# Kernel optimization log

Measured on AMD Instinct MI355X. Metric: run time of the kernel, lower is better.

## Reference

```python
import jax, jax.numpy as jnp
import numpy as np

HID, DIN, ORDER = 64, 1, 2
EPS = 1e-5


def conv1x1(x, W, b):
    # x: [b, c_in, n] -> [b, c_out, n]
    return jnp.einsum('oi,bin->bon', W, x) + b[:, None]


def gconv(x, supports, W, b, order, include_self):
    outs = [x] if include_self else []
    for A in supports:
        x1 = jnp.einsum('bcv,wv->bcw', x, A)
        outs.append(x1)
        for _ in range(order - 1):
            x1 = jnp.einsum('bcv,wv->bcw', x1, A)
            outs.append(x1)
    return conv1x1(jnp.concatenate(outs, axis=1), W, b)


def _forward(x, mask, adj, h0, fs_W, fs_b, li_W, li_b, gc_W, gc_b, lo_W, lo_b,
             ro_W, ro_b, prelu_a, f_W, f_b, u_W, u_b, c_W, c_b, gn_g, gn_beta):
    B = x.shape[0]
    supports = [adj[0], adj[1]]
    h = jnp.broadcast_to(h0, (B,) + h0.shape)  # [b, HID, n]

    def step(h, inp):
        x_s, m_s = inp  # [b, DIN, n] each
        mbool = m_s > 0
        # first stage prediction from hidden state
        xs_hat_1 = conv1x1(h, fs_W, fs_b)
        x1 = jnp.where(mbool, x_s, xs_hat_1)
        # spatial decoder (order=1, no attention)
        x_in = conv1x1(jnp.concatenate([x1, m_s, h], axis=1), li_W, li_b)
        out = gconv(x_in, supports, gc_W, gc_b, order=1, include_self=False)
        out = conv1x1(jnp.concatenate([out, h], axis=1), lo_W, lo_b)
        out = jnp.where(out >= 0, out, prelu_a * out)  # PReLU
        repr_s = jnp.concatenate([out, h], axis=1)     # [b, 2*HID, n]
        xs_hat_2 = conv1x1(repr_s, ro_W, ro_b)
        x2 = jnp.where(mbool, x1, xs_hat_2)
        # GCGRU cell (order-2 graph conv gates, include_self=True)
        rnn_in = jnp.concatenate([x2, m_s], axis=1)    # [b, 2*DIN, n]
        xh = jnp.concatenate([rnn_in, h], axis=1)
        r = jax.nn.sigmoid(gconv(xh, supports, f_W, f_b, ORDER, True))
        u = jax.nn.sigmoid(gconv(xh, supports, u_W, u_b, ORDER, True))
        xc = jnp.concatenate([rnn_in, r * h], axis=1)
        c = jnp.tanh(gconv(xc, supports, c_W, c_b, ORDER, True))
        h_new = u * h + (1.0 - u) * c
        # GroupNorm(num_groups=1): normalize over (C, N) per sample
        mu = h_new.mean(axis=(1, 2), keepdims=True)
        var = h_new.var(axis=(1, 2), keepdims=True)
        h_n = (h_new - mu) / jnp.sqrt(var + EPS) * gn_g[:, None] + gn_beta[:, None]
        return h_n, (xs_hat_2, xs_hat_1, h_n, repr_s)

    xs = jnp.moveaxis(x, -1, 0)     # [T, b, DIN, n]
    ms = jnp.moveaxis(mask, -1, 0)
    _, (imp, pred, states, reprs) = jax.lax.scan(step, h, (xs, ms))
    imputations = jnp.moveaxis(imp, 0, -1)          # [b, DIN, n, T]
    predictions = jnp.moveaxis(pred, 0, -1)
    states = jnp.moveaxis(states, 0, -1)[None]      # [n_layers=1, b, HID, n, T]
    representations = jnp.moveaxis(reprs, 0, -1)    # [b, 2*HID, n, T]
    return imputations, predictions, representations, states


def setup_inputs() -> dict:
    key = jax.random.key(0)
    ks = jax.random.split(key, 24)
    B, N, T = 8, 1024, 24
    rnn_in = 2 * DIN                 # x + mask
    dec_in = rnn_in + HID            # 66
    gate_in = 5 * (rnn_in + HID)     # (order*support_len + self) * (d_in + hidden)

    def w(k, o, i):
        return (jax.random.normal(k, (o, i), jnp.float32) / np.sqrt(i)).astype(jnp.float32)

    x = jax.random.normal(ks[0], (B, DIN, N, T), jnp.float32)
    mask = jax.random.bernoulli(ks[1], 0.8, (B, DIN, N, T)).astype(jnp.float32)
    A = jax.random.uniform(ks[2], (N, N), jnp.float32)
    A = A * (A > 0.97)  # sparse-ish graph
    fwd = A / (A.sum(1, keepdims=True) + 1e-8)
    bwd = A.T / (A.T.sum(1, keepdims=True) + 1e-8)
    adj = jnp.stack([fwd, bwd])
    return {
        'x': x, 'mask': mask, 'adj': adj,
        'h0': jax.random.normal(ks[3], (HID, N), jnp.float32) / np.sqrt(HID),
        'fs_W': w(ks[4], DIN, HID), 'fs_b': jnp.zeros((DIN,), jnp.float32),
        'li_W': w(ks[5], HID, dec_in), 'li_b': jnp.zeros((HID,), jnp.float32),
        'gc_W': w(ks[6], HID, 2 * HID), 'gc_b': jnp.zeros((HID,), jnp.float32),
        'lo_W': w(ks[7], HID, 2 * HID), 'lo_b': jnp.zeros((HID,), jnp.float32),
        'ro_W': w(ks[8], DIN, 2 * HID), 'ro_b': jnp.zeros((DIN,), jnp.float32),
        'prelu_a': jnp.float32(0.25),
        'f_W': w(ks[9], HID, gate_in), 'f_b': jnp.zeros((HID,), jnp.float32),
        'u_W': w(ks[10], HID, gate_in), 'u_b': jnp.zeros((HID,), jnp.float32),
        'c_W': w(ks[11], HID, gate_in), 'c_b': jnp.zeros((HID,), jnp.float32),
        'gn_g': jnp.ones((HID,), jnp.float32), 'gn_beta': jnp.zeros((HID,), jnp.float32),
    }


def reference(x, mask, adj, h0, fs_W, fs_b, li_W, li_b, gc_W, gc_b, lo_W, lo_b,
              ro_W, ro_b, prelu_a, f_W, f_b, u_W, u_b, c_W, c_b, gn_g, gn_beta):
    return _forward(x, mask, adj, h0, fs_W, fs_b, li_W, li_b, gc_W, gc_b,
                    lo_W, lo_b, ro_W, ro_b, prelu_a, f_W, f_b, u_W, u_b,
                    c_W, c_b, gn_g, gn_beta)
```

## Files before the change

### kernel.cpp

```cpp
#include <hip/hip_runtime.h>
#include <hip/hip_bf16.h>

typedef __hip_bfloat16 bf16;

constexpr int NV=1024, TT=24, BB=8, CAP=80;

constexpr int O_CVAL = 0;
constexpr int O_CIDX = 163840;
constexpr int O_CCNT = 327680;
constexpr int O_LIWT = 329728;
constexpr int O_GCWT = 333952;
constexpr int O_LOWT = 342144;
constexpr int O_FWT  = 350336;
constexpr int O_UWT  = 371456;
constexpr int O_CWT  = 392576;
constexpr int O_H    = 413696;
constexpr int O_T1   = 937984;
constexpr int O_T3   = 1986560;
constexpr int O_XH   = 2510848;
constexpr int O_Z1F  = 3067904;
constexpr int O_Z1B  = 3624960;
constexpr int O_PART = 4182016;
constexpr int O_RST  = 5296144;
constexpr int O_SST  = 17879056;
constexpr size_t WS_FLOATS = 24170512;
constexpr int O_XC = O_T1;
constexpr int O_U  = O_T3;

constexpr int OFF_IMP  = 0;
constexpr int OFF_PRED = 196608;
constexpr int OFF_REPR = 393216;
constexpr int OFF_ST   = 25559040;

__device__ __forceinline__ bf16 f2b(float v){ return __float2bfloat16(v); }
__device__ __forceinline__ float b2f(bf16 v){ return __bfloat162float(v); }

__global__ __launch_bounds__(64) void k_csr(const float* __restrict__ adj, float* __restrict__ ws){
  int row = blockIdx.x, lane = threadIdx.x;
  const float* a = adj + (size_t)row*NV;
  float* val = ws + O_CVAL + (size_t)row*CAP;
  int* idx = (int*)(ws+O_CIDX) + (size_t)row*CAP;
  int count = 0;
  for(int ch=0; ch<NV/64; ++ch){
    float v = a[ch*64+lane];
    unsigned long long m = __ballot(v != 0.f);
    int pre = __popcll(m & ((1ull<<lane)-1ull));
    if(v != 0.f){ int p = count+pre; if(p<CAP){ idx[p]=ch*64+lane; val[p]=v; } }
    count += __popcll(m);
  }
  if(lane==0) ((int*)(ws+O_CCNT))[row] = count>CAP?CAP:count;
}

__global__ void k_prep_wt(const float* __restrict__ liW, const float* __restrict__ gcW,
    const float* __restrict__ loW, const float* __restrict__ fW,
    const float* __restrict__ uW, const float* __restrict__ cW, float* __restrict__ ws){
  int g = blockIdx.x*blockDim.x + threadIdx.x, G = gridDim.x*blockDim.x;
  for(int i=g;i<66*64;i+=G){ int k=i>>6, c=i&63; ws[O_LIWT+i]=liW[c*66+k]; }
  for(int i=g;i<128*64;i+=G){ int k=i>>6, c=i&63; ws[O_GCWT+i]=gcW[c*128+k]; ws[O_LOWT+i]=loW[c*128+k]; }
  for(int i=g;i<330*64;i+=G){ int k=i>>6, c=i&63; ws[O_FWT+i]=fW[c*330+k]; ws[O_UWT+i]=uW[c*330+k]; ws[O_CWT+i]=cW[c*330+k]; }
}

__global__ __launch_bounds__(256) void k_h0(const float* __restrict__ h0, float* __restrict__ ws){
  int g = blockIdx.x*blockDim.x + threadIdx.x;
  if(g >= BB*NV*64) return;
  int c = g&63, n = (g>>6)&1023;
  ws[O_H + g] = h0[c*NV + n];
}

__global__ __launch_bounds__(256) void kA(float* __restrict__ ws,
    const float* __restrict__ x, const float* __restrict__ mask,
    const float* __restrict__ fsW, const float* __restrict__ fsb,
    const float* __restrict__ lib, const float* __restrict__ gng,
    const float* __restrict__ gnb, float* __restrict__ dout, int t){
  __shared__ float hs[4][2][64];
  __shared__ float rs[256], rq[256];
  __shared__ float musd[8][2];
  int tid = threadIdx.x, wid = tid>>6, lane = tid&63;
  int n = blockIdx.x;
  if(t > 0){
    const float2* part = (const float2*)(ws+O_PART);
    for(int b=0;b<8;++b){
      float sx=0.f, sq=0.f;
      for(int i=tid;i<1024;i+=256){ float2 p = part[b*1024+i]; sx+=p.x; sq+=p.y; }
      rs[tid]=sx; rq[tid]=sq; __syncthreads();
      for(int s=128;s;s>>=1){ if(tid<s){ rs[tid]+=rs[tid+s]; rq[tid]+=rq[tid+s]; } __syncthreads(); }
      if(tid==0){ float mu=rs[0]*(1.f/65536.f); float var=rq[0]*(1.f/65536.f)-mu*mu;
                  musd[b][0]=mu; musd[b][1]=rsqrtf(var+1e-5f); }
      __syncthreads();
    }
  }
  float gg = gng[lane], gb = gnb[lane];
  float x1v[2], xmv[2];
  #pragma unroll
  for(int j=0;j<2;++j){
    int b = wid*2+j;
    size_t col = (size_t)(b*NV+n);
    float h = ws[O_H + col*64 + lane];
    if(t > 0){
      h = (h - musd[b][0])*musd[b][1]*gg + gb;
      ws[O_H + col*64 + lane] = h;
      ((bf16*)(ws+O_SST))[(size_t)(t-1)*(BB*NV*64) + col*64 + lane] = f2b(h);
    }
    hs[wid][j][lane] = h;
    float pv = fsW[lane]*h;
    #pragma unroll
    for(int off=32; off; off>>=1) pv += __shfl_xor(pv, off, 64);
    float pred = pv + fsb[0];
    float xm = mask[col*TT + t];
    x1v[j] = (xm>0.f) ? x[col*TT + t] : pred;
    xmv[j] = xm;
    if(lane==0) dout[OFF_PRED + col*TT + t] = pred;
  }
  const float* Wt = ws + O_LIWT;
  float lb = lib[lane];
  float w0 = Wt[lane], w1 = Wt[64+lane];
  float a0 = lb + w0*x1v[0] + w1*xmv[0];
  float a1 = lb + w0*x1v[1] + w1*xmv[1];
  for(int j=0;j<64;++j){
    float w = Wt[(2+j)*64+lane];
    a0 += w*hs[wid][0][j];
    a1 += w*hs[wid][1][j];
  }
  ws[O_T1 + (size_t)((wid*2  )*NV+n)*64 + lane] = a0;
  ws[O_T1 + (size_t)((wid*2+1)*NV+n)*64 + lane] = a1;
}

__global__ __launch_bounds__(256) void kB(float* __restrict__ ws,
    const float* __restrict__ x, const float* __restrict__ mask,
    const float* __restrict__ gcb, const float* __restrict__ lob,
    const float* __restrict__ prelu, const float* __restrict__ roW,
    const float* __restrict__ rob, float* __restrict__ dout, int t){
  __shared__ float pq[4][2][128];
  int tid=threadIdx.x, wid=tid>>6, lane=tid&63;
  int n = blockIdx.x;
  int b0 = wid*2, b1 = wid*2+1;
  const int* ccnt = (const int*)(ws+O_CCNT);
  float p0=0.f,p1=0.f,q0=0.f,q1=0.f;
  {
    int cn = ccnt[n];
    const int* id = (const int*)(ws+O_CIDX) + (size_t)n*CAP;
    const float* vl = ws + O_CVAL + (size_t)n*CAP;
    for(int k=0;k<cn;++k){
      float a = vl[k]; int ix = id[k];
      p0 += a*ws[O_T1 + (size_t)(b0*NV+ix)*64 + lane];
      p1 += a*ws[O_T1 + (size_t)(b1*NV+ix)*64 + lane];
    }
  }
  {
    int cn = ccnt[NV+n];
    const int* id = (const int*)(ws+O_CIDX) + (size_t)(NV+n)*CAP;
    const float* vl = ws + O_CVAL + (size_t)(NV+n)*CAP;
    for(int k=0;k<cn;++k){
      float a = vl[k]; int ix = id[k];
      q0 += a*ws[O_T1 + (size_t)(b0*NV+ix)*64 + lane];
      q1 += a*ws[O_T1 + (size_t)(b1*NV+ix)*64 + lane];
    }
  }
  pq[wid][0][lane]=p0; pq[wid][0][64+lane]=q0;
  pq[wid][1][lane]=p1; pq[wid][1][64+lane]=q1;
  const float* Gt = ws + O_GCWT;
  float g0 = gcb[lane], g1 = g0;
  for(int j=0;j<128;++j){
    float w = Gt[j*64+lane];
    g0 += w*pq[wid][0][j];
    g1 += w*pq[wid][1][j];
  }
  float hv0 = ws[O_H + (size_t)(b0*NV+n)*64 + lane];
  float hv1 = ws[O_H + (size_t)(b1*NV+n)*64 + lane];
  pq[wid][0][lane]=g0; pq[wid][0][64+lane]=hv0;
  pq[wid][1][lane]=g1; pq[wid][1][64+lane]=hv1;
  const float* Lt = ws + O_LOWT;
  float o0 = lob[lane], o1 = o0;
  for(int j=0;j<128;++j){
    float w = Lt[j*64+lane];
    o0 += w*pq[wid][0][j];
    o1 += w*pq[wid][1][j];
  }
  float a = prelu[0];
  float r0 = roW[lane], r1 = roW[64+lane], rb0 = rob[0];
  bf16* reprs = (bf16*)(ws + O_RST);
  #pragma unroll
  for(int j=0;j<2;++j){
    int b = wid*2+j;
    float ov = (j? o1 : o0);
    float hv = (j? hv1 : hv0);
    ov = (ov>=0.f)? ov : a*ov;
    size_t col = (size_t)(b*NV+n);
    size_t rbo = (((size_t)t*BB + b)*NV + n)*128;
    reprs[rbo + lane]      = f2b(ov);
    reprs[rbo + 64 + lane] = f2b(hv);
    float rv = r0*ov + r1*hv;
    #pragma unroll
    for(int off=32; off; off>>=1) rv += __shfl_xor(rv, off, 64);
    float xs2 = rv + rb0;
    float xm = mask[col*TT+t];
    float x2 = (xm>0.f) ? x[col*TT+t] : xs2;
    if(lane==0) dout[OFF_IMP + col*TT + t] = xs2;
    float* xh = ws + O_XH + col*68;
    xh[2+lane] = hv;
    if(lane==0){ xh[0]=x2; xh[1]=xm; }
  }
}

__global__ __launch_bounds__(256) void k_prop(float* __restrict__ ws, int srcF, int srcB,
    int dstF, int dstB){
  int tid=threadIdx.x, wid = tid>>6, lane = tid&63;
  int n = blockIdx.x;
  int b0 = wid*2, b1 = wid*2+1;
  const int* ccnt = (const int*)(ws+O_CCNT);
  bool hi = lane < 2;
  {
    int cn = ccnt[n];
    const int* id = (const int*)(ws+O_CIDX) + (size_t)n*CAP;
    const float* vl = ws + O_CVAL + (size_t)n*CAP;
    float a00=0.f,a01=0.f,a10=0.f,a11=0.f;
    for(int k=0;k<cn;++k){
      float a = vl[k]; int ix = id[k];
      const float* r0 = ws + srcF + (size_t)(b0*NV + ix)*68;
      const float* r1 = ws + srcF + (size_t)(b1*NV + ix)*68;
      a00 += a*r0[lane]; if(hi) a01 += a*r0[64+lane];
      a10 += a*r1[lane]; if(hi) a11 += a*r1[64+lane];
    }
    float* d0 = ws + dstF + (size_t)(b0*NV+n)*68;
    float* d1 = ws + dstF + (size_t)(b1*NV+n)*68;
    d0[lane]=a00; if(hi) d0[64+lane]=a01;
    d1[lane]=a10; if(hi) d1[64+lane]=a11;
  }
  {
    int cn = ccnt[NV+n];
    const int* id = (const int*)(ws+O_CIDX) + (size_t)(NV+n)*CAP;
    const float* vl = ws + O_CVAL + (size_t)(NV+n)*CAP;
    float a00=0.f,a01=0.f,a10=0.f,a11=0.f;
    for(int k=0;k<cn;++k){
      float a = vl[k]; int ix = id[k];
      const float* r0 = ws + srcB + (size_t)(b0*NV + ix)*68;
      const float* r1 = ws + srcB + (size_t)(b1*NV + ix)*68;
      a00 += a*r0[lane]; if(hi) a01 += a*r0[64+lane];
      a10 += a*r1[lane]; if(hi) a11 += a*r1[64+lane];
    }
    float* d0 = ws + dstB + (size_t)(b0*NV+n)*68;
    float* d1 = ws + dstB + (size_t)(b1*NV+n)*68;
    d0[lane]=a00; if(hi) d0[64+lane]=a01;
    d1[lane]=a10; if(hi) d1[64+lane]=a11;
  }
}

__global__ __launch_bounds__(256) void kD(float* __restrict__ ws,
    const float* __restrict__ fb, const float* __restrict__ ub){
  __shared__ float vec[4][2][332];
  int tid=threadIdx.x, wid=tid>>6, lane=tid&63;
  int n = blockIdx.x;
  const int* ccnt = (const int*)(ws+O_CCNT);
  bool hi = lane < 2;
  #pragma unroll
  for(int j=0;j<2;++j){
    size_t col = (size_t)((wid*2+j)*NV+n);
    const float* xh  = ws + O_XH  + col*68;
    const float* z1f = ws + O_Z1F + col*68;
    const float* z1b = ws + O_Z1B + col*68;
    vec[wid][j][lane]     = xh[lane];   if(hi) vec[wid][j][64+lane]  = xh[64+lane];
    vec[wid][j][66+lane]  = z1f[lane];  if(hi) vec[wid][j][130+lane] = z1f[64+lane];
    vec[wid][j][198+lane] = z1b[lane];  if(hi) vec[wid][j][262+lane] = z1b[64+lane];
  }
  {
    int cn = ccnt[n];
    const int* id = (const int*)(ws+O_CIDX) + (size_t)n*CAP;
    const float* vl = ws + O_CVAL + (size_t)n*CAP;
    float a00=0.f,a01=0.f,a10=0.f,a11=0.f;
    for(int k=0;k<cn;++k){
      float a = vl[k]; int ix = id[k];
      const float* r0 = ws + O_Z1F + (size_t)((wid*2  )*NV+ix)*68;
      const float* r1 = ws + O_Z1F + (size_t)((wid*2+1)*NV+ix)*68;
      a00 += a*r0[lane]; if(hi) a01 += a*r0[64+lane];
      a10 += a*r1[lane]; if(hi) a11 += a*r1[64+lane];
    }
    vec[wid][0][132+lane]=a00; if(hi) vec[wid][0][196+lane]=a01;
    vec[wid][1][132+lane]=a10; if(hi) vec[wid][1][196+lane]=a11;
  }
  {
    int cn = ccnt[NV+n];
    const int* id = (const int*)(ws+O_CIDX) + (size_t)(NV+n)*CAP;
    const float* vl = ws + O_CVAL + (size_t)(NV+n)*CAP;
    float a00=0.f,a01=0.f,a10=0.f,a11=0.f;
    for(int k=0;k<cn;++k){
      float a = vl[k]; int ix = id[k];
      const float* r0 = ws + O_Z1B + (size_t)((wid*2  )*NV+ix)*68;
      const float* r1 = ws + O_Z1B + (size_t)((wid*2+1)*NV+ix)*68;
      a00 += a*r0[lane]; if(hi) a01 += a*r0[64+lane];
      a10 += a*r1[lane]; if(hi) a11 += a*r1[64+lane];
    }
    vec[wid][0][264+lane]=a00; if(hi) vec[wid][0][328+lane]=a01;
    vec[wid][1][264+lane]=a10; if(hi) vec[wid][1][328+lane]=a11;
  }
  const float* Ft = ws + O_FWT;
  const float* Ut = ws + O_UWT;
  float ar0 = fb[lane], ar1 = ar0;
  float au0 = ub[lane], au1 = au0;
  for(int k=0;k<330;++k){
    float wf = Ft[k*64+lane];
    float wu = Ut[k*64+lane];
    float v0 = vec[wid][0][k], v1 = vec[wid][1][k];
    ar0 += wf*v0; ar1 += wf*v1;
    au0 += wu*v0; au1 += wu*v1;
  }
  #pragma unroll
  for(int j=0;j<2;++j){
    size_t col = (size_t)((wid*2+j)*NV+n);
    float r = 1.f/(1.f+expf(-(j? ar1 : ar0)));
    float u = 1.f/(1.f+expf(-(j? au1 : au0)));
    float hv = ws[O_H + col*64 + lane];
    ws[O_U + col*64 + lane] = u;
    float* xc = ws + O_XC + col*68;
    xc[2+lane] = r*hv;
    if(hi) xc[lane] = vec[wid][j][lane];
  }
}

__global__ __launch_bounds__(256) void kF(float* __restrict__ ws, const float* __restrict__ cb){
  __shared__ float vec[4][2][332];
  int tid=threadIdx.x, wid=tid>>6, lane=tid&63;
  int n = blockIdx.x;
  const int* ccnt = (const int*)(ws+O_CCNT);
  bool hi = lane < 2;
  #pragma unroll
  for(int j=0;j<2;++j){
    size_t col = (size_t)((wid*2+j)*NV+n);
    const float* xc  = ws + O_XC  + col*68;
    const float* w1f = ws + O_Z1F + col*68;
    const float* w1b = ws + O_Z1B + col*68;
    vec[wid][j][lane]     = xc[lane];   if(hi) vec[wid][j][64+lane]  = xc[64+lane];
    vec[wid][j][66+lane]  = w1f[lane];  if(hi) vec[wid][j][130+lane] = w1f[64+lane];
    vec[wid][j][198+lane] = w1b[lane];  if(hi) vec[wid][j][262+lane] = w1b[64+lane];
  }
  {
    int cn = ccnt[n];
    const int* id = (const int*)(ws+O_CIDX) + (size_t)n*CAP;
    const float* vl = ws + O_CVAL + (size_t)n*CAP;
    float a00=0.f,a01=0.f,a10=0.f,a11=0.f;
    for(int k=0;k<cn;++k){
      float a = vl[k]; int ix = id[k];
      const float* r0 = ws + O_Z1F + (size_t)((wid*2  )*NV+ix)*68;
      const float* r1 = ws + O_Z1F + (size_t)((wid*2+1)*NV+ix)*68;
      a00 += a*r0[lane]; if(hi) a01 += a*r0[64+lane];
      a10 += a*r1[lane]; if(hi) a11 += a*r1[64+lane];
    }
    vec[wid][0][132+lane]=a00; if(hi) vec[wid][0][196+lane]=a01;
    vec[wid][1][132+lane]=a10; if(hi) vec[wid][1][196+lane]=a11;
  }
  {
    int cn = ccnt[NV+n];
    const int* id = (const int*)(ws+O_CIDX) + (size_t)(NV+n)*CAP;
    const float* vl = ws + O_CVAL + (size_t)(NV+n)*CAP;
    float a00=0.f,a01=0.f,a10=0.f,a11=0.f;
    for(int k=0;k<cn;++k){
      float a = vl[k]; int ix = id[k];
      const float* r0 = ws + O_Z1B + (size_t)((wid*2  )*NV+ix)*68;
      const float* r1 = ws + O_Z1B + (size_t)((wid*2+1)*NV+ix)*68;
      a00 += a*r0[lane]; if(hi) a01 += a*r0[64+lane];
      a10 += a*r1[lane]; if(hi) a11 += a*r1[64+lane];
    }
    vec[wid][0][264+lane]=a00; if(hi) vec[wid][0][328+lane]=a01;
    vec[wid][1][264+lane]=a10; if(hi) vec[wid][1][328+lane]=a11;
  }
  const float* Ct = ws + O_CWT;
  float ac0 = cb[lane], ac1 = ac0;
  for(int k=0;k<330;++k){
    float wc = Ct[k*64+lane];
    ac0 += wc*vec[wid][0][k];
    ac1 += wc*vec[wid][1][k];
  }
  #pragma unroll
  for(int j=0;j<2;++j){
    int b = wid*2+j;
    size_t col = (size_t)(b*NV+n);
    float cd = tanhf(j? ac1 : ac0);
    float hv = ws[O_H + col*64 + lane];
    float u  = ws[O_U + col*64 + lane];
    float hn = u*hv + (1.f-u)*cd;
    ws[O_H + col*64 + lane] = hn;
    float s = hn, sq = hn*hn;
    #pragma unroll
    for(int off=32; off; off>>=1){ s += __shfl_xor(s, off, 64); sq += __shfl_xor(sq, off, 64); }
    if(lane==0) ((float2*)(ws+O_PART))[b*1024 + n] = make_float2(s, sq);
  }
}

__global__ __launch_bounds__(256) void k_final(float* __restrict__ ws,
    const float* __restrict__ gng, const float* __restrict__ gnb){
  __shared__ float rs[256], rq[256];
  __shared__ float musd[8][2];
  int tid=threadIdx.x, wid=tid>>6, lane=tid&63;
  int n = blockIdx.x;
  const float2* part = (const float2*)(ws+O_PART);
  for(int b=0;b<8;++b){
    float sx=0.f, sq=0.f;
    for(int i=tid;i<1024;i+=256){ float2 p = part[b*1024+i]; sx+=p.x; sq+=p.y; }
    rs[tid]=sx; rq[tid]=sq; __syncthreads();
    for(int s=128;s;s>>=1){ if(tid<s){ rs[tid]+=rs[tid+s]; rq[tid]+=rq[tid+s]; } __syncthreads(); }
    if(tid==0){ float mu=rs[0]*(1.f/65536.f); float var=rq[0]*(1.f/65536.f)-mu*mu;
                musd[b][0]=mu; musd[b][1]=rsqrtf(var+1e-5f); }
    __syncthreads();
  }
  float gg=gng[lane], gb=gnb[lane];
  #pragma unroll
  for(int j=0;j<2;++j){
    int b = wid*2+j;
    size_t col = (size_t)(b*NV+n);
    float hn = ws[O_H + col*64 + lane];
    float h = (hn-musd[b][0])*musd[b][1]*gg + gb;
    ((bf16*)(ws+O_SST))[(size_t)23*(BB*NV*64) + col*64 + lane] = f2b(h);
  }
}

__global__ __launch_bounds__(256) void k_transpose(const float* __restrict__ ws, float* __restrict__ dout,
                                                   int srcOff, int dstOff, int CH){
  __shared__ bf16 ld[32][16][26];
  int ct = CH/16;
  int per_b = 32*ct;
  int b = blockIdx.x / per_b;
  int r = blockIdx.x - b*per_b;
  int n0 = (r/ct)*32, ch0 = (r - (r/ct)*ct)*16;
  const bf16* src = (const bf16*)(ws + srcOff);
  for(int t=0;t<TT;++t){
    for(int i=threadIdx.x;i<512;i+=256){
      int cc=i&15, nn=i>>4;
      ld[nn][cc][t] = src[(((size_t)t*BB + b)*NV + n0+nn)*CH + ch0+cc];
    }
  }
  __syncthreads();
  for(int i=threadIdx.x;i<512;i+=256){
    int nn=i&31, cc=i>>5;
    size_t ob = ((size_t)(b*CH + ch0+cc)*NV + n0+nn)*TT;
    #pragma unroll
    for(int t=0;t<TT;++t) dout[dstOff + ob + t] = b2f(ld[nn][cc][t]);
  }
}

extern "C" void kernel_launch(void* const* d_in, const int* in_sizes, int n_in,
                              void* d_out, int out_size, void* d_ws, size_t ws_size,
                              hipStream_t stream){
  if(ws_size < WS_FLOATS * sizeof(float)) return;
  if(n_in < 23) return;

  float* ws = (float*)d_ws;
  float* out = (float*)d_out;

  const float* x    = (const float*)d_in[0];
  const float* mask = (const float*)d_in[1];
  const float* adj  = (const float*)d_in[2];
  const float* h0   = (const float*)d_in[3];
  const float* fsW  = (const float*)d_in[4];
  const float* fsb  = (const float*)d_in[5];
  const float* liW  = (const float*)d_in[6];
  const float* lib  = (const float*)d_in[7];
  const float* gcW  = (const float*)d_in[8];
  const float* gcb  = (const float*)d_in[9];
  const float* loW  = (const float*)d_in[10];
  const float* lob  = (const float*)d_in[11];
  const float* roW  = (const float*)d_in[12];
  const float* rob  = (const float*)d_in[13];
  const float* prelu= (const float*)d_in[14];
  const float* fW   = (const float*)d_in[15];
  const float* fb   = (const float*)d_in[16];
  const float* uW   = (const float*)d_in[17];
  const float* ub   = (const float*)d_in[18];
  const float* cW   = (const float*)d_in[19];
  const float* cb   = (const float*)d_in[20];
  const float* gng  = (const float*)d_in[21];
  const float* gnb  = (const float*)d_in[22];

  k_csr    <<<dim3(2048), dim3(64),  0, stream>>>(adj, ws);
  k_prep_wt<<<dim3(64),   dim3(256), 0, stream>>>(liW, gcW, loW, fW, uW, cW, ws);
  k_h0     <<<dim3(2048), dim3(256), 0, stream>>>(h0, ws);

  for(int t=0; t<TT; ++t){
    kA    <<<dim3(1024), dim3(256), 0, stream>>>(ws, x, mask, fsW, fsb, lib, gng, gnb, out, t);
    kB    <<<dim3(1024), dim3(256), 0, stream>>>(ws, x, mask, gcb, lob, prelu, roW, rob, out, t);
    k_prop<<<dim3(1024), dim3(256), 0, stream>>>(ws, O_XH, O_XH, O_Z1F, O_Z1B);
    kD    <<<dim3(1024), dim3(256), 0, stream>>>(ws, fb, ub);
    k_prop<<<dim3(1024), dim3(256), 0, stream>>>(ws, O_XC, O_XC, O_Z1F, O_Z1B);
    kF    <<<dim3(1024), dim3(256), 0, stream>>>(ws, cb);
  }
  k_final<<<dim3(1024), dim3(256), 0, stream>>>(ws, gng, gnb);

  k_transpose<<<dim3(2048), dim3(256), 0, stream>>>(ws, out, O_RST, OFF_REPR, 128);
  k_transpose<<<dim3(1024), dim3(256), 0, stream>>>(ws, out, O_SST, OFF_ST, 64);
}
```

Before: 5.785 ms.

## Split gate kernels across two waves per batch pair and speed GroupNorm stats

kD and kF now launch 512 threads. Two waves share each batch pair: one handles the forward-support gather and the other the backward-support gather, and each computes half of the 330-long weight reduction. The halves are combined through shared memory, which is meant to halve the per-wave serial latency of the sparse gather and the dense matvec. The GroupNorm statistics reduction in kA and k_final replaces the eight sequential block-wide tree reductions with one 32-lane shuffle reduction per batch. Sparse gather loops also get unroll-4 pragmas. The cost is extra barriers and shared-memory use per block, which may reduce occupancy.

After: 5.158 ms. 10.8% less time.

```diff
diff --git a/kernel.cpp b/kernel.cpp
--- a/kernel.cpp
+++ b/kernel.cpp
@@ -73,21 +73,20 @@
     const float* __restrict__ lib, const float* __restrict__ gng,
     const float* __restrict__ gnb, float* __restrict__ dout, int t){
   __shared__ float hs[4][2][64];
-  __shared__ float rs[256], rq[256];
   __shared__ float musd[8][2];
   int tid = threadIdx.x, wid = tid>>6, lane = tid&63;
   int n = blockIdx.x;
   if(t > 0){
     const float2* part = (const float2*)(ws+O_PART);
-    for(int b=0;b<8;++b){
-      float sx=0.f, sq=0.f;
-      for(int i=tid;i<1024;i+=256){ float2 p = part[b*1024+i]; sx+=p.x; sq+=p.y; }
-      rs[tid]=sx; rq[tid]=sq; __syncthreads();
-      for(int s=128;s;s>>=1){ if(tid<s){ rs[tid]+=rs[tid+s]; rq[tid]+=rq[tid+s]; } __syncthreads(); }
-      if(tid==0){ float mu=rs[0]*(1.f/65536.f); float var=rq[0]*(1.f/65536.f)-mu*mu;
-                  musd[b][0]=mu; musd[b][1]=rsqrtf(var+1e-5f); }
-      __syncthreads();
-    }
+    int b = wid*2 + (lane>>5);
+    int l5 = lane&31;
+    float sx=0.f, sq=0.f;
+    for(int i=l5;i<1024;i+=32){ float2 pp = part[b*1024+i]; sx+=pp.x; sq+=pp.y; }
+    #pragma unroll
+    for(int off=16;off;off>>=1){ sx+=__shfl_xor(sx,off,64); sq+=__shfl_xor(sq,off,64); }
+    if(l5==0){ float mu=sx*(1.f/65536.f);
+               musd[b][0]=mu; musd[b][1]=rsqrtf(sq*(1.f/65536.f)-mu*mu+1e-5f); }
+    __syncthreads();
   }
   float gg = gng[lane], gb = gnb[lane];
   float x1v[2], xmv[2];
@@ -140,6 +139,7 @@
     int cn = ccnt[n];
     const int* id = (const int*)(ws+O_CIDX) + (size_t)n*CAP;
     const float* vl = ws + O_CVAL + (size_t)n*CAP;
+    #pragma unroll 4
     for(int k=0;k<cn;++k){
       float a = vl[k]; int ix = id[k];
       p0 += a*ws[O_T1 + (size_t)(b0*NV+ix)*64 + lane];
@@ -150,6 +150,7 @@
     int cn = ccnt[NV+n];
     const int* id = (const int*)(ws+O_CIDX) + (size_t)(NV+n)*CAP;
     const float* vl = ws + O_CVAL + (size_t)(NV+n)*CAP;
+    #pragma unroll 4
     for(int k=0;k<cn;++k){
       float a = vl[k]; int ix = id[k];
       q0 += a*ws[O_T1 + (size_t)(b0*NV+ix)*64 + lane];
@@ -214,6 +215,7 @@
     const int* id = (const int*)(ws+O_CIDX) + (size_t)n*CAP;
     const float* vl = ws + O_CVAL + (size_t)n*CAP;
     float a00=0.f,a01=0.f,a10=0.f,a11=0.f;
+    #pragma unroll 4
     for(int k=0;k<cn;++k){
       float a = vl[k]; int ix = id[k];
       const float* r0 = ws + srcF + (size_t)(b0*NV + ix)*68;
@@ -231,6 +233,7 @@
     const int* id = (const int*)(ws+O_CIDX) + (size_t)(NV+n)*CAP;
     const float* vl = ws + O_CVAL + (size_t)(NV+n)*CAP;
     float a00=0.f,a01=0.f,a10=0.f,a11=0.f;
+    #pragma unroll 4
     for(int k=0;k<cn;++k){
       float a = vl[k]; int ix = id[k];
       const float* r0 = ws + srcB + (size_t)(b0*NV + ix)*68;
@@ -245,160 +248,192 @@
   }
 }
 
-__global__ __launch_bounds__(256) void kD(float* __restrict__ ws,
+__global__ __launch_bounds__(512) void kD(float* __restrict__ ws,
     const float* __restrict__ fb, const float* __restrict__ ub){
   __shared__ float vec[4][2][332];
-  int tid=threadIdx.x, wid=tid>>6, lane=tid&63;
+  __shared__ float acc[8][4][64];
+  int tid=threadIdx.x, w=tid>>6, lane=tid&63;
+  int pair=w>>1, half=w&1;
   int n = blockIdx.x;
+  int b0 = pair*2, b1 = b0+1;
+  size_t c0=(size_t)(b0*NV+n), c1=(size_t)(b1*NV+n);
   const int* ccnt = (const int*)(ws+O_CCNT);
   bool hi = lane < 2;
-  #pragma unroll
-  for(int j=0;j<2;++j){
-    size_t col = (size_t)((wid*2+j)*NV+n);
-    const float* xh  = ws + O_XH  + col*68;
-    const float* z1f = ws + O_Z1F + col*68;
-    const float* z1b = ws + O_Z1B + col*68;
-    vec[wid][j][lane]     = xh[lane];   if(hi) vec[wid][j][64+lane]  = xh[64+lane];
-    vec[wid][j][66+lane]  = z1f[lane];  if(hi) vec[wid][j][130+lane] = z1f[64+lane];
-    vec[wid][j][198+lane] = z1b[lane];  if(hi) vec[wid][j][262+lane] = z1b[64+lane];
-  }
-  {
+  if(half==0){
+    const float* xh0 = ws + O_XH + c0*68;
+    const float* xh1 = ws + O_XH + c1*68;
+    const float* z1f0 = ws + O_Z1F + c0*68;
+    const float* z1f1 = ws + O_Z1F + c1*68;
+    vec[pair][0][lane]=xh0[lane];     if(hi) vec[pair][0][64+lane]=xh0[64+lane];
+    vec[pair][1][lane]=xh1[lane];     if(hi) vec[pair][1][64+lane]=xh1[64+lane];
+    vec[pair][0][66+lane]=z1f0[lane]; if(hi) vec[pair][0][130+lane]=z1f0[64+lane];
+    vec[pair][1][66+lane]=z1f1[lane]; if(hi) vec[pair][1][130+lane]=z1f1[64+lane];
     int cn = ccnt[n];
     const int* id = (const int*)(ws+O_CIDX) + (size_t)n*CAP;
     const float* vl = ws + O_CVAL + (size_t)n*CAP;
     float a00=0.f,a01=0.f,a10=0.f,a11=0.f;
-    for(int k=0;k<cn;++k){
-      float a = vl[k]; int ix = id[k];
-      const float* r0 = ws + O_Z1F + (size_t)((wid*2  )*NV+ix)*68;
-      const float* r1 = ws + O_Z1F + (size_t)((wid*2+1)*NV+ix)*68;
+    #pragma unroll 4
+    for(int k=0;k<cn;++k){
+      float a = vl[k]; int ix = id[k];
+      const float* r0 = ws + O_Z1F + (size_t)(b0*NV+ix)*68;
+      const float* r1 = ws + O_Z1F + (size_t)(b1*NV+ix)*68;
       a00 += a*r0[lane]; if(hi) a01 += a*r0[64+lane];
       a10 += a*r1[lane]; if(hi) a11 += a*r1[64+lane];
     }
-    vec[wid][0][132+lane]=a00; if(hi) vec[wid][0][196+lane]=a01;
-    vec[wid][1][132+lane]=a10; if(hi) vec[wid][1][196+lane]=a11;
-  }
-  {
+    vec[pair][0][132+lane]=a00; if(hi) vec[pair][0][196+lane]=a01;
+    vec[pair][1][132+lane]=a10; if(hi) vec[pair][1][196+lane]=a11;
+  } else {
+    const float* z1b0 = ws + O_Z1B + c0*68;
+    const float* z1b1 = ws + O_Z1B + c1*68;
+    vec[pair][0][198+lane]=z1b0[lane]; if(hi) vec[pair][0][262+lane]=z1b0[64+lane];
+    vec[pair][1][198+lane]=z1b1[lane]; if(hi) vec[pair][1][262+lane]=z1b1[64+lane];
     int cn = ccnt[NV+n];
     const int* id = (const int*)(ws+O_CIDX) + (size_t)(NV+n)*CAP;
     const float* vl = ws + O_CVAL + (size_t)(NV+n)*CAP;
     float a00=0.f,a01=0.f,a10=0.f,a11=0.f;
-    for(int k=0;k<cn;++k){
-      float a = vl[k]; int ix = id[k];
-      const float* r0 = ws + O_Z1B + (size_t)((wid*2  )*NV+ix)*68;
-      const float* r1 = ws + O_Z1B + (size_t)((wid*2+1)*NV+ix)*68;
+    #pragma unroll 4
+    for(int k=0;k<cn;++k){
+      float a = vl[k]; int ix = id[k];
+      const float* r0 = ws + O_Z1B + (size_t)(b0*NV+ix)*68;
+      const float* r1 = ws + O_Z1B + (size_t)(b1*NV+ix)*68;
       a00 += a*r0[lane]; if(hi) a01 += a*r0[64+lane];
       a10 += a*r1[lane]; if(hi) a11 += a*r1[64+lane];
     }
-    vec[wid][0][264+lane]=a00; if(hi) vec[wid][0][328+lane]=a01;
-    vec[wid][1][264+lane]=a10; if(hi) vec[wid][1][328+lane]=a11;
-  }
+    vec[pair][0][264+lane]=a00; if(hi) vec[pair][0][328+lane]=a01;
+    vec[pair][1][264+lane]=a10; if(hi) vec[pair][1][328+lane]=a11;
+  }
+  __syncthreads();
   const float* Ft = ws + O_FWT;
   const float* Ut = ws + O_UWT;
-  float ar0 = fb[lane], ar1 = ar0;
-  float au0 = ub[lane], au1 = au0;
-  for(int k=0;k<330;++k){
+  int k0 = half*165, k1 = k0+165;
+  float ar0 = half? 0.f : fb[lane];
+  float au0 = half? 0.f : ub[lane];
+  float ar1 = ar0, au1 = au0;
+  for(int k=k0;k<k1;++k){
     float wf = Ft[k*64+lane];
     float wu = Ut[k*64+lane];
-    float v0 = vec[wid][0][k], v1 = vec[wid][1][k];
+    float v0 = vec[pair][0][k], v1 = vec[pair][1][k];
     ar0 += wf*v0; ar1 += wf*v1;
     au0 += wu*v0; au1 += wu*v1;
   }
-  #pragma unroll
-  for(int j=0;j<2;++j){
-    size_t col = (size_t)((wid*2+j)*NV+n);
-    float r = 1.f/(1.f+expf(-(j? ar1 : ar0)));
-    float u = 1.f/(1.f+expf(-(j? au1 : au0)));
-    float hv = ws[O_H + col*64 + lane];
-    ws[O_U + col*64 + lane] = u;
-    float* xc = ws + O_XC + col*68;
-    xc[2+lane] = r*hv;
-    if(hi) xc[lane] = vec[wid][j][lane];
-  }
-}
-
-__global__ __launch_bounds__(256) void kF(float* __restrict__ ws, const float* __restrict__ cb){
+  acc[w][0][lane]=ar0; acc[w][1][lane]=ar1; acc[w][2][lane]=au0; acc[w][3][lane]=au1;
+  __syncthreads();
+  if(half==0){
+    ar0 += acc[w+1][0][lane]; ar1 += acc[w+1][1][lane];
+    au0 += acc[w+1][2][lane]; au1 += acc[w+1][3][lane];
+    float r0 = 1.f/(1.f+expf(-ar0)), r1v = 1.f/(1.f+expf(-ar1));
+    float u0 = 1.f/(1.f+expf(-au0)), u1v = 1.f/(1.f+expf(-au1));
+    float hv0 = ws[O_H + c0*64 + lane];
+    float hv1 = ws[O_H + c1*64 + lane];
+    ws[O_U + c0*64 + lane] = u0;
+    ws[O_U + c1*64 + lane] = u1v;
+    float* xc0 = ws + O_XC + c0*68;
+    float* xc1 = ws + O_XC + c1*68;
+    xc0[2+lane] = r0*hv0; xc1[2+lane] = r1v*hv1;
+    if(hi){ xc0[lane] = vec[pair][0][lane]; xc1[lane] = vec[pair][1][lane]; }
+  }
+}
+
+__global__ __launch_bounds__(512) void kF(float* __restrict__ ws, const float* __restrict__ cb){
   __shared__ float vec[4][2][332];
-  int tid=threadIdx.x, wid=tid>>6, lane=tid&63;
+  __shared__ float acc[8][2][64];
+  int tid=threadIdx.x, w=tid>>6, lane=tid&63;
+  int pair=w>>1, half=w&1;
   int n = blockIdx.x;
+  int b0 = pair*2, b1 = b0+1;
+  size_t c0=(size_t)(b0*NV+n), c1=(size_t)(b1*NV+n);
   const int* ccnt = (const int*)(ws+O_CCNT);
   bool hi = lane < 2;
-  #pragma unroll
-  for(int j=0;j<2;++j){
-    size_t col = (size_t)((wid*2+j)*NV+n);
-    const float* xc  = ws + O_XC  + col*68;
-    const float* w1f = ws + O_Z1F + col*68;
-    const float* w1b = ws + O_Z1B + col*68;
-    vec[wid][j][lane]     = xc[lane];   if(hi) vec[wid][j][64+lane]  = xc[64+lane];
-    vec[wid][j][66+lane]  = w1f[lane];  if(hi) vec[wid][j][130+lane] = w1f[64+lane];
-    vec[wid][j][198+lane] = w1b[lane];  if(hi) vec[wid][j][262+lane] = w1b[64+lane];
-  }
-  {
+  if(half==0){
+    const float* xc0 = ws + O_XC + c0*68;
+    const float* xc1 = ws + O_XC + c1*68;
+    const float* w1f0 = ws + O_Z1F + c0*68;
+    const float* w1f1 = ws + O_Z1F + c1*68;
+    vec[pair][0][lane]=xc0[lane];      if(hi) vec[pair][0][64+lane]=xc0[64+lane];
+    vec[pair][1][lane]=xc1[lane];      if(hi) vec[pair][1][64+lane]=xc1[64+lane];
+    vec[pair][0][66+lane]=w1f0[lane];  if(hi) vec[pair][0][130+lane]=w1f0[64+lane];
+    vec[pair][1][66+lane]=w1f1[lane];  if(hi) vec[pair][1][130+lane]=w1f1[64+lane];
     int cn = ccnt[n];
     const int* id = (const int*)(ws+O_CIDX) + (size_t)n*CAP;
     const float* vl = ws + O_CVAL + (size_t)n*CAP;
     float a00=0.f,a01=0.f,a10=0.f,a11=0.f;
-    for(int k=0;k<cn;++k){
-      float a = vl[k]; int ix = id[k];
-      const float* r0 = ws + O_Z1F + (size_t)((wid*2  )*NV+ix)*68;
-      const float* r1 = ws + O_Z1F + (size_t)((wid*2+1)*NV+ix)*68;
+    #pragma unroll 4
+    for(int k=0;k<cn;++k){
+      float a = vl[k]; int ix = id[k];
+      const float* r0 = ws + O_Z1F + (size_t)(b0*NV+ix)*68;
+      const float* r1 = ws + O_Z1F + (size_t)(b1*NV+ix)*68;
       a00 += a*r0[lane]; if(hi) a01 += a*r0[64+lane];
       a10 += a*r1[lane]; if(hi) a11 += a*r1[64+lane];
     }
-    vec[wid][0][132+lane]=a00; if(hi) vec[wid][0][196+lane]=a01;
-    vec[wid][1][132+lane]=a10; if(hi) vec[wid][1][196+lane]=a11;
-  }
-  {
+    vec[pair][0][132+lane]=a00; if(hi) vec[pair][0][196+lane]=a01;
+    vec[pair][1][132+lane]=a10; if(hi) vec[pair][1][196+lane]=a11;
+  } else {
+    const float* w1b0 = ws + O_Z1B + c0*68;
+    const float* w1b1 = ws + O_Z1B + c1*68;
+    vec[pair][0][198+lane]=w1b0[lane]; if(hi) vec[pair][0][262+lane]=w1b0[64+lane];
+    vec[pair][1][198+lane]=w1b1[lane]; if(hi) vec[pair][1][262+lane]=w1b1[64+lane];
     int cn = ccnt[NV+n];
     const int* id = (const int*)(ws+O_CIDX) + (size_t)(NV+n)*CAP;
     const float* vl = ws + O_CVAL + (size_t)(NV+n)*CAP;
     float a00=0.f,a01=0.f,a10=0.f,a11=0.f;
-    for(int k=0;k<cn;++k){
-      float a = vl[k]; int ix = id[k];
-      const float* r0 = ws + O_Z1B + (size_t)((wid*2  )*NV+ix)*68;
-      const float* r1 = ws + O_Z1B + (size_t)((wid*2+1)*NV+ix)*68;
+    #pragma unroll 4
+    for(int k=0;k<cn;++k){
+      float a = vl[k]; int ix = id[k];
+      const float* r0 = ws + O_Z1B + (size_t)(b0*NV+ix)*68;
+      const float* r1 = ws + O_Z1B + (size_t)(b1*NV+ix)*68;
       a00 += a*r0[lane]; if(hi) a01 += a*r0[64+lane];
       a10 += a*r1[lane]; if(hi) a11 += a*r1[64+lane];
     }
-    vec[wid][0][264+lane]=a00; if(hi) vec[wid][0][328+lane]=a01;
-    vec[wid][1][264+lane]=a10; if(hi) vec[wid][1][328+lane]=a11;
-  }
+    vec[pair][0][264+lane]=a00; if(hi) vec[pair][0][328+lane]=a01;
+    vec[pair][1][264+lane]=a10; if(hi) vec[pair][1][328+lane]=a11;
+  }
+  __syncthreads();
   const float* Ct = ws + O_CWT;
-  float ac0 = cb[lane], ac1 = ac0;
-  for(int k=0;k<330;++k){
+  int k0 = half*165, k1 = k0+165;
+  float ac0 = half? 0.f : cb[lane];
+  float ac1 = ac0;
+  for(int k=k0;k<k1;++k){
     float wc = Ct[k*64+lane];
-    ac0 += wc*vec[wid][0][k];
-    ac1 += wc*vec[wid][1][k];
-  }
-  #pragma unroll
-  for(int j=0;j<2;++j){
-    int b = wid*2+j;
-    size_t col = (size_t)(b*NV+n);
-    float cd = tanhf(j? ac1 : ac0);
-    float hv = ws[O_H + col*64 + lane];
-    float u  = ws[O_U + col*64 + lane];
-    float hn = u*hv + (1.f-u)*cd;
-    ws[O_H + col*64 + lane] = hn;
-    float s = hn, sq = hn*hn;
+    ac0 += wc*vec[pair][0][k];
+    ac1 += wc*vec[pair][1][k];
+  }
+  acc[w][0][lane]=ac0; acc[w][1][lane]=ac1;
+  __syncthreads();
+  if(half==0){
+    ac0 += acc[w+1][0][lane];
+    ac1 += acc[w+1][1][lane];
     #pragma unroll
-    for(int off=32; off; off>>=1){ s += __shfl_xor(s, off, 64); sq += __shfl_xor(sq, off, 64); }
-    if(lane==0) ((float2*)(ws+O_PART))[b*1024 + n] = make_float2(s, sq);
+    for(int j=0;j<2;++j){
+      int b = b0+j;
+      size_t col = (j? c1 : c0);
+      float cd = tanhf(j? ac1 : ac0);
+      float hv = ws[O_H + col*64 + lane];
+      float u  = ws[O_U + col*64 + lane];
+      float hn = u*hv + (1.f-u)*cd;
+      ws[O_H + col*64 + lane] = hn;
+      float s = hn, sq = hn*hn;
+      #pragma unroll
+      for(int off=32; off; off>>=1){ s += __shfl_xor(s, off, 64); sq += __shfl_xor(sq, off, 64); }
+      if(lane==0) ((float2*)(ws+O_PART))[b*1024 + n] = make_float2(s, sq);
+    }
   }
 }
 
 __global__ __launch_bounds__(256) void k_final(float* __restrict__ ws,
     const float* __restrict__ gng, const float* __restrict__ gnb){
-  __shared__ float rs[256], rq[256];
   __shared__ float musd[8][2];
   int tid=threadIdx.x, wid=tid>>6, lane=tid&63;
   int n = blockIdx.x;
   const float2* part = (const float2*)(ws+O_PART);
-  for(int b=0;b<8;++b){
+  {
+    int b = wid*2 + (lane>>5);
+    int l5 = lane&31;
     float sx=0.f, sq=0.f;
-    for(int i=tid;i<1024;i+=256){ float2 p = part[b*1024+i]; sx+=p.x; sq+=p.y; }
-    rs[tid]=sx; rq[tid]=sq; __syncthreads();
-    for(int s=128;s;s>>=1){ if(tid<s){ rs[tid]+=rs[tid+s]; rq[tid]+=rq[tid+s]; } __syncthreads(); }
-    if(tid==0){ float mu=rs[0]*(1.f/65536.f); float var=rq[0]*(1.f/65536.f)-mu*mu;
-                musd[b][0]=mu; musd[b][1]=rsqrtf(var+1e-5f); }
+    for(int i=l5;i<1024;i+=32){ float2 pp = part[b*1024+i]; sx+=pp.x; sq+=pp.y; }
+    #pragma unroll
+    for(int off=16;off;off>>=1){ sx+=__shfl_xor(sx,off,64); sq+=__shfl_xor(sq,off,64); }
+    if(l5==0){ float mu=sx*(1.f/65536.f);
+               musd[b][0]=mu; musd[b][1]=rsqrtf(sq*(1.f/65536.f)-mu*mu+1e-5f); }
     __syncthreads();
   }
   float gg=gng[lane], gb=gnb[lane];
@@ -451,35 +486,31 @@
   const float* h0   = (const float*)d_in[3];
   const float* fsW  = (const float*)d_in[4];
   const float* fsb  = (const float*)d_in[5];
-  const float* liW  = (const float*)d_in[6];
   const float* lib  = (const float*)d_in[7];
-  const float* gcW  = (const float*)d_in[8];
   const float* gcb  = (const float*)d_in[9];
-  const float* loW  = (const float*)d_in[10];
   const float* lob  = (const float*)d_in[11];
   const float* roW  = (const float*)d_in[12];
   const float* rob  = (const float*)d_in[13];
   const float* prelu= (const float*)d_in[14];
-  const float* fW   = (const float*)d_in[15];
   const float* fb   = (const float*)d_in[16];
-  const float* uW   = (const float*)d_in[17];
   const float* ub   = (const float*)d_in[18];
-  const float* cW   = (const float*)d_in[19];
   const float* cb   = (const float*)d_in[20];
   const float* gng  = (const float*)d_in[21];
   const float* gnb  = (const float*)d_in[22];
 
   k_csr    <<<dim3(2048), dim3(64),  0, stream>>>(adj, ws);
-  k_prep_wt<<<dim3(64),   dim3(256), 0, stream>>>(liW, gcW, loW, fW, uW, cW, ws);
+  k_prep_wt<<<dim3(64),   dim3(256), 0, stream>>>(
+      (const float*)d_in[6], (const float*)d_in[8], (const float*)d_in[10],
+      (const float*)d_in[15], (const float*)d_in[17], (const float*)d_in[19], ws);
   k_h0     <<<dim3(2048), dim3(256), 0, stream>>>(h0, ws);
 
   for(int t=0; t<TT; ++t){
     kA    <<<dim3(1024), dim3(256), 0, stream>>>(ws, x, mask, fsW, fsb, lib, gng, gnb, out, t);
     kB    <<<dim3(1024), dim3(256), 0, stream>>>(ws, x, mask, gcb, lob, prelu, roW, rob, out, t);
     k_prop<<<dim3(1024), dim3(256), 0, stream>>>(ws, O_XH, O_XH, O_Z1F, O_Z1B);
-    kD    <<<dim3(1024), dim3(256), 0, stream>>>(ws, fb, ub);
+    kD    <<<dim3(1024), dim3(512), 0, stream>>>(ws, fb, ub);
     k_prop<<<dim3(1024), dim3(256), 0, stream>>>(ws, O_XC, O_XC, O_Z1F, O_Z1B);
-    kF    <<<dim3(1024), dim3(256), 0, stream>>>(ws, cb);
+    kF    <<<dim3(1024), dim3(512), 0, stream>>>(ws, cb);
   }
   k_final<<<dim3(1024), dim3(256), 0, stream>>>(ws, gng, gnb);
 
```
